# Kernel optimization log

Hardware: AMD Instinct MI355X
Metric: run time of the kernel (lower is better)

Reference implementation:

```python
import jax, jax.numpy as jnp
import numpy as np

EMBED_DIM = 528
NUM_HEADS = 8
HEAD_DIM = EMBED_DIM // NUM_HEADS  # 66


def setup_inputs() -> dict:
    key = jax.random.key(0)
    k1, k2, k3, k4, k5 = jax.random.split(key, 5)
    B, D, H, W, C = 1, 16, 16, 16, EMBED_DIM
    s = 1.0 / np.sqrt(C)
    return {
        "x": jax.random.normal(k1, (B, D, H, W, C), dtype=jnp.float32),
        "w_qkv": jax.random.uniform(k2, (3 * C, C), dtype=jnp.float32, minval=-s, maxval=s),
        "b_qkv": jax.random.uniform(k3, (3 * C,), dtype=jnp.float32, minval=-s, maxval=s),
        "w_proj": jax.random.uniform(k4, (C, C), dtype=jnp.float32, minval=-s, maxval=s),
        "b_proj": jax.random.uniform(k5, (C,), dtype=jnp.float32, minval=-s, maxval=s),
    }


def reference(x, w_qkv, b_qkv, w_proj, b_proj):
    B, D, H, W, C = x.shape
    N = D * H * W
    h, hd = NUM_HEADS, HEAD_DIM
    scaling = hd ** (-0.5)

    xt = x.reshape(B, N, C)
    # qkv projection: [B, N, 3C] -> [3, B, h, N, hd]
    qkv = xt @ w_qkv.T + b_qkv
    qkv = qkv.reshape(B, N, 3, h, hd).transpose(2, 0, 3, 1, 4)
    q, k, v = qkv[0], qkv[1], qkv[2]

    # full attention over all D*H*W tokens
    attn = jnp.einsum('bhqd,bhkd->bhqk', q, k) * scaling
    attn = jax.nn.softmax(attn, axis=-1)
    out = jnp.einsum('bhqk,bhkd->bhqd', attn, v)  # [B, h, N, hd]

    out = out.transpose(0, 2, 1, 3).reshape(B, N, h * hd)
    out = out @ w_proj.T + b_proj
    return out.reshape(B, D, H, W, C)
```

## Files before the change

### kernel.cpp

```cpp
#include <hip/hip_runtime.h>

typedef __attribute__((ext_vector_type(8))) short bf16x8;
typedef __attribute__((ext_vector_type(4))) float f32x4;
typedef __attribute__((ext_vector_type(16))) float f32x16;

#define DEV __device__ __forceinline__

static constexpr int N_TOK = 4096;
static constexpr int C     = 528;
static constexpr int NH    = 8;
static constexpr int HD    = 66;
static constexpr int HDP   = 96;
static constexpr int VD96  = 96;
static constexpr int KP    = 544;
static constexpr int NQKV  = 1584;
static constexpr int NQKVP = 1632;

DEV unsigned short f2bf(float f) {
    unsigned int u = __float_as_uint(f);
    u = (u + 0x7fffu + ((u >> 16) & 1u)) >> 16;
    return (unsigned short)u;
}
DEV float bf2f(unsigned short h) { return __uint_as_float(((unsigned int)h) << 16); }
DEV unsigned cvtpk2(float a, float b) {
    unsigned r;
    asm("v_cvt_pk_bf16_f32 %0, %1, %2" : "=v"(r) : "v"(a), "v"(b));
    return r;
}
DEV void plswap(unsigned &a, unsigned &b) {
    asm volatile("v_permlane32_swap_b32 %0, %1" : "+v"(a), "+v"(b));
}

__global__ void k_prep_all(const float* __restrict__ x, const float* __restrict__ w_qkv,
                           const float* __restrict__ w_proj,
                           unsigned short* __restrict__ xb, unsigned short* __restrict__ wqkvb,
                           unsigned short* __restrict__ whi, unsigned short* __restrict__ wlo,
                           unsigned short* __restrict__ qb, unsigned short* __restrict__ kbuf) {
    const int T0 = N_TOK * KP;
    const int T1 = T0 + NQKVP * KP;
    const int T2 = T1 + KP * KP;
    const int T3 = T2 + NH * N_TOK * (HDP - HD);
    for (int idx = blockIdx.x * 256 + threadIdx.x; idx < T3; idx += gridDim.x * 256) {
        if (idx < T0) {
            int n = idx / KP, k = idx - n * KP;
            xb[idx] = (k < C) ? f2bf(x[n * C + k]) : (unsigned short)0;
        } else if (idx < T1) {
            int j = idx - T0;
            int n = j / KP, k = j - n * KP;
            wqkvb[j] = (n < NQKV && k < C) ? f2bf(w_qkv[n * C + k]) : (unsigned short)0;
        } else if (idx < T2) {
            int j = idx - T1;
            int n = j / KP, k = j - n * KP;
            unsigned short hi = 0, lo = 0;
            if (n < C && k < C) {
                float v = w_proj[n * C + k];
                hi = f2bf(v);
                lo = f2bf(v - bf2f(hi));
            }
            whi[j] = hi; wlo[j] = lo;
        } else {
            int j = idx - T2;
            int n = j / 30, p = j - 30 * n;
            size_t a = (size_t)n * HDP + HD + p;
            qb[a] = 0; kbuf[a] = 0;
        }
    }
}

__launch_bounds__(256)
__global__ void k_gemm_qkv(const unsigned short* __restrict__ A,
                           const unsigned short* __restrict__ B,
                           const float* __restrict__ bias,
                           unsigned short* __restrict__ qb, unsigned short* __restrict__ kbuf,
                           unsigned short* __restrict__ vtmp) {
    constexpr int LDA = 40;
    __shared__ unsigned short Al[2][128 * LDA];
    __shared__ unsigned short Bl[2][96 * LDA];
    int tid = threadIdx.x, lane = tid & 63, wid = tid >> 6;
    int m0 = blockIdx.x * 128, n0 = blockIdx.y * 96;
    int wm = (wid >> 1) * 64, wn = (wid & 1) * 48;
    int arow0 = tid >> 2, arow1 = (256 + tid) >> 2, akc = (tid & 3) * 8;
    bool bhave = tid < 128;
    int brow1 = (256 + tid) >> 2;
    f32x4 acc[4][3] = {};
    bf16x8 ra0, ra1, rb0, rb1;

    ra0 = *(const bf16x8*)&A[(size_t)(m0 + arow0) * KP + akc];
    ra1 = *(const bf16x8*)&A[(size_t)(m0 + arow1) * KP + akc];
    rb0 = *(const bf16x8*)&B[(size_t)(n0 + arow0) * KP + akc];
    if (bhave) rb1 = *(const bf16x8*)&B[(size_t)(n0 + brow1) * KP + akc];
    *(bf16x8*)&Al[0][arow0 * LDA + akc] = ra0;
    *(bf16x8*)&Al[0][arow1 * LDA + akc] = ra1;
    *(bf16x8*)&Bl[0][arow0 * LDA + akc] = rb0;
    if (bhave) *(bf16x8*)&Bl[0][brow1 * LDA + akc] = rb1;
    __syncthreads();

    int kk = (lane >> 4) * 8, cc = lane & 15;
    for (int kt = 0; kt < 17; kt++) {
        int cur = kt & 1;
        if (kt < 16) {
            int k0 = (kt + 1) * 32;
            ra0 = *(const bf16x8*)&A[(size_t)(m0 + arow0) * KP + k0 + akc];
            ra1 = *(const bf16x8*)&A[(size_t)(m0 + arow1) * KP + k0 + akc];
            rb0 = *(const bf16x8*)&B[(size_t)(n0 + arow0) * KP + k0 + akc];
            if (bhave) rb1 = *(const bf16x8*)&B[(size_t)(n0 + brow1) * KP + k0 + akc];
        }
        bf16x8 af[4], bfr[3];
#pragma unroll
        for (int mi = 0; mi < 4; mi++) af[mi] = *(const bf16x8*)&Al[cur][(wm + mi * 16 + cc) * LDA + kk];
#pragma unroll
        for (int ni = 0; ni < 3; ni++) bfr[ni] = *(const bf16x8*)&Bl[cur][(wn + ni * 16 + cc) * LDA + kk];
#pragma unroll
        for (int mi = 0; mi < 4; mi++)
#pragma unroll
            for (int ni = 0; ni < 3; ni++)
                acc[mi][ni] = __builtin_amdgcn_mfma_f32_16x16x32_bf16(af[mi], bfr[ni], acc[mi][ni], 0, 0, 0);
        if (kt < 16) {
            int nxt = cur ^ 1;
            *(bf16x8*)&Al[nxt][arow0 * LDA + akc] = ra0;
            *(bf16x8*)&Al[nxt][arow1 * LDA + akc] = ra1;
            *(bf16x8*)&Bl[nxt][arow0 * LDA + akc] = rb0;
            if (bhave) *(bf16x8*)&Bl[nxt][brow1 * LDA + akc] = rb1;
        }
        __syncthreads();
    }
#pragma unroll
    for (int mi = 0; mi < 4; mi++)
#pragma unroll
        for (int ni = 0; ni < 3; ni++)
#pragma unroll
            for (int r = 0; r < 4; r++) {
                int row = m0 + wm + mi * 16 + (lane >> 4) * 4 + r;
                int col = n0 + wn + ni * 16 + cc;
                float v = acc[mi][ni][r] + (col < NQKV ? bias[col] : 0.f);
                unsigned short b = f2bf(v);
                if (col < 2 * C) {
                    int d5 = (col >= C) ? col - C : col;
                    unsigned h = (unsigned)d5 / 66u;
                    int dd = d5 - 66 * (int)h;
                    size_t a = ((size_t)h * N_TOK + row) * HDP + dd;
                    if (col >= C) kbuf[a] = b; else qb[a] = b;
                } else if (col < NQKV) {
                    vtmp[(size_t)row * C + (col - 2 * C)] = b;
                }
            }
}

__global__ void k_reshape_v(const unsigned short* __restrict__ vtmp, unsigned short* __restrict__ vt) {
    __shared__ unsigned short lt[64 * 104];
    int h = blockIdx.y, n0 = blockIdx.x * 64, tid = threadIdx.x;
#pragma unroll
    for (int i = 0; i < 24; i++) {
        int idx = i * 256 + tid;
        int ni = idx / 96, d = idx - ni * 96;
        unsigned short v = 0;
        if (d < HD) v = vtmp[(size_t)(n0 + ni) * C + h * HD + d];
        lt[ni * 104 + d] = v;
    }
    __syncthreads();
#pragma unroll
    for (int i = 0; i < 24; i++) {
        int idx = i * 256 + tid;
        int d = idx >> 6, ni = idx & 63;
        vt[((size_t)h * VD96 + d) * N_TOK + n0 + ni] = lt[ni * 104 + d];
    }
}

__launch_bounds__(512, 2)
__global__ void k_attn(const unsigned short* __restrict__ qb,
                       const unsigned short* __restrict__ kb,
                       const unsigned short* __restrict__ vt,
                       unsigned short* __restrict__ ahi,
                       unsigned short* __restrict__ alo) {
    __shared__ __align__(16) unsigned short S[128 * 128 + 96 * 128];
    int tid = threadIdx.x, lane = tid & 63, wid = tid >> 6;
    int wq = wid & 3;
    int kh = wid >> 2;
    int hi = lane >> 5, lq = lane & 31;
    int bid = blockIdx.x;
    int head = bid & 7;
    int q0 = (bid >> 3) * 128;
    const float SC2 = 0.12309149097933274f * 1.4426950408889634f;

    bf16x8 aq[6];
    {
        const unsigned short* qrow = qb + ((size_t)head * N_TOK + q0 + wq * 32 + lq) * HDP + hi * 8;
#pragma unroll
        for (int t = 0; t < 6; t++) aq[t] = *(const bf16x8*)&qrow[t * 16];
    }
    f32x16 o0 = {}, o1 = {}, o2 = {};
    float m_r = -3e38f, l_r = 0.f;

    const unsigned short* kg = kb + (size_t)head * N_TOK * HDP;
    const unsigned short* vg = vt + (size_t)head * VD96 * N_TOK;

    const unsigned short* gpK[3];
    const unsigned short* gpV[3];
    int laK[3], laV[3];
#pragma unroll
    for (int j = 0; j < 3; j++) {
        int c = j * 512 + tid;
        int row = c / 12, ch = c - row * 12;
        gpK[j] = kg + (size_t)row * HDP + ch * 8;
        laK[j] = row * 128 + ((ch ^ (row & 15)) << 3);
        int row2 = c >> 4, ch2 = c & 15;
        gpV[j] = vg + (size_t)row2 * N_TOK + ch2 * 8;
        laV[j] = 128 * 128 + row2 * 128 + ((ch2 ^ (row2 & 15)) << 3);
    }
#pragma unroll
    for (int j = 0; j < 3; j++) {
        *(bf16x8*)&S[laK[j]] = *(const bf16x8*)gpK[j];
        *(bf16x8*)&S[laV[j]] = *(const bf16x8*)gpV[j];
    }
    __syncthreads();

    for (int kt = 0; kt < 32; kt++) {
        bf16x8 gk[3], gv[3];
        if (kt < 31) {
            size_t n1 = (size_t)(kt + 1) * 128;
#pragma unroll
            for (int j = 0; j < 3; j++) {
                gk[j] = *(const bf16x8*)(gpK[j] + n1 * HDP);
                gv[j] = *(const bf16x8*)(gpV[j] + n1);
            }
        }

        f32x16 s0 = {}, s1 = {};
        {
            int r0 = kh * 64 + lq, r1 = r0 + 32;
#pragma unroll
            for (int t = 0; t < 6; t++) {
                bf16x8 ka0 = *(const bf16x8*)&S[r0 * 128 + (((2 * t + hi) ^ (r0 & 15)) << 3)];
                bf16x8 ka1 = *(const bf16x8*)&S[r1 * 128 + (((2 * t + hi) ^ (r1 & 15)) << 3)];
                s0 = __builtin_amdgcn_mfma_f32_32x32x16_bf16(ka0, aq[t], s0, 0, 0, 0);
                s1 = __builtin_amdgcn_mfma_f32_32x32x16_bf16(ka1, aq[t], s1, 0, 0, 0);
            }
        }

        float mx = s0[0];
#pragma unroll
        for (int r = 1; r < 16; r++) mx = fmaxf(mx, s0[r]);
#pragma unroll
        for (int r = 0; r < 16; r++) mx = fmaxf(mx, s1[r]);
        mx = fmaxf(mx, __shfl_xor(mx, 32, 64));
        if (!__all((mx - m_r) * SC2 <= 8.f)) {
            float mnew = fmaxf(m_r, mx);
            float fct = __builtin_amdgcn_exp2f((m_r - mnew) * SC2);
            m_r = mnew;
            l_r *= fct;
#pragma unroll
            for (int r = 0; r < 16; r++) { o0[r] *= fct; o1[r] *= fct; o2[r] *= fct; }
        }
        float nb = m_r * SC2;
        float lsum = 0.f;
#pragma unroll
        for (int r = 0; r < 16; r++) { s0[r] = __builtin_amdgcn_exp2f(__builtin_fmaf(s0[r], SC2, -nb)); lsum += s0[r]; }
#pragma unroll
        for (int r = 0; r < 16; r++) { s1[r] = __builtin_amdgcn_exp2f(__builtin_fmaf(s1[r], SC2, -nb)); lsum += s1[r]; }
        lsum += __shfl_xor(lsum, 32, 64);
        l_r += lsum;

        unsigned u0[2][4], u1[2][4];
#pragma unroll
        for (int a = 0; a < 4; a++) {
            u0[0][a] = cvtpk2(s0[4 * a + 0], s0[4 * a + 1]);
            u1[0][a] = cvtpk2(s0[4 * a + 2], s0[4 * a + 3]);
            u0[1][a] = cvtpk2(s1[4 * a + 0], s1[4 * a + 1]);
            u1[1][a] = cvtpk2(s1[4 * a + 2], s1[4 * a + 3]);
        }
#pragma unroll
        for (int kb2 = 0; kb2 < 2; kb2++)
#pragma unroll
            for (int a0 = 0; a0 < 4; a0 += 2) {
                plswap(u0[kb2][a0], u0[kb2][a0 + 1]);
                plswap(u1[kb2][a0], u1[kb2][a0 + 1]);
            }

#pragma unroll
        for (int t2 = 0; t2 < 4; t2++) {
            int kb2 = t2 >> 1, a0 = (t2 & 1) * 2;
            union { unsigned u[4]; bf16x8 v; } pf;
            pf.u[0] = u0[kb2][a0];     pf.u[1] = u1[kb2][a0];
            pf.u[2] = u0[kb2][a0 + 1]; pf.u[3] = u1[kb2][a0 + 1];
            int ch = kh * 8 + 2 * t2 + hi;
            int rv0 = lq, rv1 = 32 + lq, rv2 = 64 + lq;
            bf16x8 va0 = *(const bf16x8*)&S[128 * 128 + rv0 * 128 + ((ch ^ (rv0 & 15)) << 3)];
            bf16x8 va1 = *(const bf16x8*)&S[128 * 128 + rv1 * 128 + ((ch ^ (rv1 & 15)) << 3)];
            bf16x8 va2 = *(const bf16x8*)&S[128 * 128 + rv2 * 128 + ((ch ^ (rv2 & 15)) << 3)];
            o0 = __builtin_amdgcn_mfma_f32_32x32x16_bf16(va0, pf.v, o0, 0, 0, 0);
            o1 = __builtin_amdgcn_mfma_f32_32x32x16_bf16(va1, pf.v, o1, 0, 0, 0);
            o2 = __builtin_amdgcn_mfma_f32_32x32x16_bf16(va2, pf.v, o2, 0, 0, 0);
        }

        __syncthreads();
        if (kt < 31) {
#pragma unroll
            for (int j = 0; j < 3; j++) {
                *(bf16x8*)&S[laK[j]] = gk[j];
                *(bf16x8*)&S[laV[j]] = gv[j];
            }
        }
        __syncthreads();
    }

    float* xc = (float*)&S[0];
    float* rg = xc + (size_t)((wq * 64 + lane) * 52);
    if (kh == 1) {
#pragma unroll
        for (int r = 0; r < 16; r++) { rg[r] = o0[r]; rg[16 + r] = o1[r]; rg[32 + r] = o2[r]; }
        rg[48] = m_r; rg[49] = l_r;
    }
    __syncthreads();
    if (kh == 0) {
        float m1 = rg[48], l1 = rg[49];
        float m12 = fmaxf(m_r, m1);
        float f0 = __builtin_amdgcn_exp2f((m_r - m12) * SC2);
        float f1 = __builtin_amdgcn_exp2f((m1 - m12) * SC2);
        float inv = 1.f / (l_r * f0 + l1 * f1);
        int token = q0 + wq * 32 + lq;
#pragma unroll
        for (int db = 0; db < 3; db++) {
#pragma unroll
            for (int r = 0; r < 16; r++) {
                int d = db * 32 + (r & 3) + 8 * (r >> 2) + 4 * hi;
                if (d < HD) {
                    float own = (db == 0) ? o0[r] : (db == 1) ? o1[r] : o2[r];
                    float val = (own * f0 + rg[db * 16 + r] * f1) * inv;
                    unsigned short hb = f2bf(val);
                    float lo = val - bf2f(hb);
                    size_t a = (size_t)token * KP + head * HD + d;
                    ahi[a] = hb; alo[a] = f2bf(lo);
                }
            }
        }
    }
}

__launch_bounds__(256)
__global__ void k_gemm_proj(const unsigned short* __restrict__ Ahi_, const unsigned short* __restrict__ Alo_,
                            const unsigned short* __restrict__ Whi_, const unsigned short* __restrict__ Wlo_,
                            const float* __restrict__ bias, float* __restrict__ out) {
    constexpr int LDA = 40;
    __shared__ unsigned short Ah[2][128 * LDA], Aw[2][128 * LDA];
    __shared__ unsigned short Bh[2][64 * LDA],  Bw[2][64 * LDA];
    int tid = threadIdx.x, lane = tid & 63, wid = tid >> 6;
    int m0 = blockIdx.x * 128, n0 = blockIdx.y * 64;
    int wm = wid * 32;
    int arow0 = tid >> 2, arow1 = (256 + tid) >> 2, akc = (tid & 3) * 8;
    bool bok = (n0 + arow0) < KP;
    f32x4 acc[2][4] = {};
    bf16x8 rah0, rah1, ral0, ral1, rbh, rbl;
    const bf16x8 zero8 = {};

    rah0 = *(const bf16x8*)&Ahi_[(size_t)(m0 + arow0) * KP + akc];
    rah1 = *(const bf16x8*)&Ahi_[(size_t)(m0 + arow1) * KP + akc];
    ral0 = *(const bf16x8*)&Alo_[(size_t)(m0 + arow0) * KP + akc];
    ral1 = *(const bf16x8*)&Alo_[(size_t)(m0 + arow1) * KP + akc];
    rbh = bok ? *(const bf16x8*)&Whi_[(size_t)(n0 + arow0) * KP + akc] : zero8;
    rbl = bok ? *(const bf16x8*)&Wlo_[(size_t)(n0 + arow0) * KP + akc] : zero8;
    *(bf16x8*)&Ah[0][arow0 * LDA + akc] = rah0;
    *(bf16x8*)&Ah[0][arow1 * LDA + akc] = rah1;
    *(bf16x8*)&Aw[0][arow0 * LDA + akc] = ral0;
    *(bf16x8*)&Aw[0][arow1 * LDA + akc] = ral1;
    *(bf16x8*)&Bh[0][arow0 * LDA + akc] = rbh;
    *(bf16x8*)&Bw[0][arow0 * LDA + akc] = rbl;
    __syncthreads();

    int kk = (lane >> 4) * 8, cc = lane & 15;
    for (int kt = 0; kt < 17; kt++) {
        int cur = kt & 1;
        if (kt < 16) {
            int k0 = (kt + 1) * 32;
            rah0 = *(const bf16x8*)&Ahi_[(size_t)(m0 + arow0) * KP + k0 + akc];
            rah1 = *(const bf16x8*)&Ahi_[(size_t)(m0 + arow1) * KP + k0 + akc];
            ral0 = *(const bf16x8*)&Alo_[(size_t)(m0 + arow0) * KP + k0 + akc];
            ral1 = *(const bf16x8*)&Alo_[(size_t)(m0 + arow1) * KP + k0 + akc];
            rbh = bok ? *(const bf16x8*)&Whi_[(size_t)(n0 + arow0) * KP + k0 + akc] : zero8;
            rbl = bok ? *(const bf16x8*)&Wlo_[(size_t)(n0 + arow0) * KP + k0 + akc] : zero8;
        }
        bf16x8 ah[2], al[2], bh[4], bl[4];
#pragma unroll
        for (int mi = 0; mi < 2; mi++) {
            ah[mi] = *(const bf16x8*)&Ah[cur][(wm + mi * 16 + cc) * LDA + kk];
            al[mi] = *(const bf16x8*)&Aw[cur][(wm + mi * 16 + cc) * LDA + kk];
        }
#pragma unroll
        for (int ni = 0; ni < 4; ni++) {
            bh[ni] = *(const bf16x8*)&Bh[cur][(ni * 16 + cc) * LDA + kk];
            bl[ni] = *(const bf16x8*)&Bw[cur][(ni * 16 + cc) * LDA + kk];
        }
#pragma unroll
        for (int mi = 0; mi < 2; mi++)
#pragma unroll
            for (int ni = 0; ni < 4; ni++) {
                acc[mi][ni] = __builtin_amdgcn_mfma_f32_16x16x32_bf16(ah[mi], bh[ni], acc[mi][ni], 0, 0, 0);
                acc[mi][ni] = __builtin_amdgcn_mfma_f32_16x16x32_bf16(ah[mi], bl[ni], acc[mi][ni], 0, 0, 0);
                acc[mi][ni] = __builtin_amdgcn_mfma_f32_16x16x32_bf16(al[mi], bh[ni], acc[mi][ni], 0, 0, 0);
            }
        if (kt < 16) {
            int nxt = cur ^ 1;
            *(bf16x8*)&Ah[nxt][arow0 * LDA + akc] = rah0;
            *(bf16x8*)&Ah[nxt][arow1 * LDA + akc] = rah1;
            *(bf16x8*)&Aw[nxt][arow0 * LDA + akc] = ral0;
            *(bf16x8*)&Aw[nxt][arow1 * LDA + akc] = ral1;
            *(bf16x8*)&Bh[nxt][arow0 * LDA + akc] = rbh;
            *(bf16x8*)&Bw[nxt][arow0 * LDA + akc] = rbl;
        }
        __syncthreads();
    }
#pragma unroll
    for (int mi = 0; mi < 2; mi++)
#pragma unroll
        for (int ni = 0; ni < 4; ni++)
#pragma unroll
            for (int r = 0; r < 4; r++) {
                int row = m0 + wm + mi * 16 + (lane >> 4) * 4 + r;
                int col = n0 + ni * 16 + cc;
                if (col < C) out[(size_t)row * C + col] = acc[mi][ni][r] + bias[col];
            }
}

extern "C" void kernel_launch(void* const* d_in, const int* in_sizes, int n_in,
                              void* d_out, int out_size, void* d_ws, size_t ws_size,
                              hipStream_t stream) {
    const float* x      = (const float*)d_in[0];
    const float* w_qkv  = (const float*)d_in[1];
    const float* b_qkv  = (const float*)d_in[2];
    const float* w_proj = (const float*)d_in[3];
    const float* b_proj = (const float*)d_in[4];
    float* out = (float*)d_out;
    char* ws = (char*)d_ws;

    const size_t o_xb    = 0;
    const size_t o_wqkvb = o_xb    + 4456448;
    const size_t o_whi   = o_wqkvb + 1775616;
    const size_t o_wlo   = o_whi   + 591872;
    const size_t o_vtmp  = o_wlo   + 591872;
    const size_t o_qbf   = o_vtmp  + 4456448;
    const size_t o_kbf   = o_qbf   + 6291456;
    const size_t o_vt    = o_kbf   + 6291456;
    const size_t need    = o_vt + 6291456;
    if (ws_size < need) return;

    unsigned short* xb    = (unsigned short*)(ws + o_xb);
    unsigned short* wqkvb = (unsigned short*)(ws + o_wqkvb);
    unsigned short* whi   = (unsigned short*)(ws + o_whi);
    unsigned short* wlo   = (unsigned short*)(ws + o_wlo);
    unsigned short* vtmp  = (unsigned short*)(ws + o_vtmp);
    unsigned short* qbf   = (unsigned short*)(ws + o_qbf);
    unsigned short* kbf   = (unsigned short*)(ws + o_kbf);
    unsigned short* vt    = (unsigned short*)(ws + o_vt);
    unsigned short* ahi   = xb;
    unsigned short* alo   = vtmp;

    k_prep_all  <<<2048, 256, 0, stream>>>(x, w_qkv, w_proj, xb, wqkvb, whi, wlo, qbf, kbf);
    k_gemm_qkv  <<<dim3(N_TOK / 128, NQKVP / 96), 256, 0, stream>>>(xb, wqkvb, b_qkv, qbf, kbf, vtmp);
    k_reshape_v <<<dim3(N_TOK / 64, NH), 256, 0, stream>>>(vtmp, vt);
    k_attn      <<<dim3(256), 512, 0, stream>>>(qbf, kbf, vt, ahi, alo);
    k_gemm_proj <<<dim3(N_TOK / 128, 9), 256, 0, stream>>>(ahi, alo, whi, wlo, b_proj, out);
}
```

Baseline: 129.4 us.

## Split attention keys four ways per block with 1024 threads and 256-key tiles

The attention kernel now launches 1024-thread blocks in which four wave groups each cover a quarter of every 256-key tile, instead of two groups on 128-key tiles. The loop runs 16 iterations instead of 32, which halves the number of barrier pairs and doubles the waves resident per CU, giving more latency hiding. The partial softmax states are merged in two rounds through LDS. In exchange, LDS use grows to about 112 KB and per-thread register limits stay tight at 1024 threads.

```diff
diff --git a/kernel.cpp b/kernel.cpp
--- a/kernel.cpp
+++ b/kernel.cpp
@@ -166,13 +166,14 @@
     }
 }
 
-__launch_bounds__(512, 2)
+__launch_bounds__(1024, 1)
 __global__ void k_attn(const unsigned short* __restrict__ qb,
                        const unsigned short* __restrict__ kb,
                        const unsigned short* __restrict__ vt,
                        unsigned short* __restrict__ ahi,
                        unsigned short* __restrict__ alo) {
-    __shared__ __align__(16) unsigned short S[128 * 128 + 96 * 128];
+    __shared__ __align__(16) unsigned short S[256 * 128 + 96 * 256];
+    constexpr int VOFF = 256 * 128;
     int tid = threadIdx.x, lane = tid & 63, wid = tid >> 6;
     int wq = wid & 3;
     int kh = wid >> 2;
@@ -199,13 +200,13 @@
     int laK[3], laV[3];
 #pragma unroll
     for (int j = 0; j < 3; j++) {
-        int c = j * 512 + tid;
+        int c = j * 1024 + tid;
         int row = c / 12, ch = c - row * 12;
         gpK[j] = kg + (size_t)row * HDP + ch * 8;
         laK[j] = row * 128 + ((ch ^ (row & 15)) << 3);
-        int row2 = c >> 4, ch2 = c & 15;
+        int row2 = c >> 5, ch2 = c & 31;
         gpV[j] = vg + (size_t)row2 * N_TOK + ch2 * 8;
-        laV[j] = 128 * 128 + row2 * 128 + ((ch2 ^ (row2 & 15)) << 3);
+        laV[j] = VOFF + row2 * 256 + ((ch2 ^ (row2 & 15)) << 3);
     }
 #pragma unroll
     for (int j = 0; j < 3; j++) {
@@ -214,10 +215,10 @@
     }
     __syncthreads();
 
-    for (int kt = 0; kt < 32; kt++) {
+    for (int kt = 0; kt < 16; kt++) {
         bf16x8 gk[3], gv[3];
-        if (kt < 31) {
-            size_t n1 = (size_t)(kt + 1) * 128;
+        if (kt < 15) {
+            size_t n1 = (size_t)(kt + 1) * 256;
 #pragma unroll
             for (int j = 0; j < 3; j++) {
                 gk[j] = *(const bf16x8*)(gpK[j] + n1 * HDP);
@@ -284,16 +285,16 @@
             pf.u[2] = u0[kb2][a0 + 1]; pf.u[3] = u1[kb2][a0 + 1];
             int ch = kh * 8 + 2 * t2 + hi;
             int rv0 = lq, rv1 = 32 + lq, rv2 = 64 + lq;
-            bf16x8 va0 = *(const bf16x8*)&S[128 * 128 + rv0 * 128 + ((ch ^ (rv0 & 15)) << 3)];
-            bf16x8 va1 = *(const bf16x8*)&S[128 * 128 + rv1 * 128 + ((ch ^ (rv1 & 15)) << 3)];
-            bf16x8 va2 = *(const bf16x8*)&S[128 * 128 + rv2 * 128 + ((ch ^ (rv2 & 15)) << 3)];
+            bf16x8 va0 = *(const bf16x8*)&S[VOFF + rv0 * 256 + ((ch ^ (rv0 & 15)) << 3)];
+            bf16x8 va1 = *(const bf16x8*)&S[VOFF + rv1 * 256 + ((ch ^ (rv1 & 15)) << 3)];
+            bf16x8 va2 = *(const bf16x8*)&S[VOFF + rv2 * 256 + ((ch ^ (rv2 & 15)) << 3)];
             o0 = __builtin_amdgcn_mfma_f32_32x32x16_bf16(va0, pf.v, o0, 0, 0, 0);
             o1 = __builtin_amdgcn_mfma_f32_32x32x16_bf16(va1, pf.v, o1, 0, 0, 0);
             o2 = __builtin_amdgcn_mfma_f32_32x32x16_bf16(va2, pf.v, o2, 0, 0, 0);
         }
 
         __syncthreads();
-        if (kt < 31) {
+        if (kt < 15) {
 #pragma unroll
             for (int j = 0; j < 3; j++) {
                 *(bf16x8*)&S[laK[j]] = gk[j];
@@ -304,32 +305,58 @@
     }
 
     float* xc = (float*)&S[0];
-    float* rg = xc + (size_t)((wq * 64 + lane) * 52);
-    if (kh == 1) {
-#pragma unroll
-        for (int r = 0; r < 16; r++) { rg[r] = o0[r]; rg[16 + r] = o1[r]; rg[32 + r] = o2[r]; }
-        rg[48] = m_r; rg[49] = l_r;
-    }
-    __syncthreads();
-    if (kh == 0) {
-        float m1 = rg[48], l1 = rg[49];
-        float m12 = fmaxf(m_r, m1);
-        float f0 = __builtin_amdgcn_exp2f((m_r - m12) * SC2);
-        float f1 = __builtin_amdgcn_exp2f((m1 - m12) * SC2);
-        float inv = 1.f / (l_r * f0 + l1 * f1);
-        int token = q0 + wq * 32 + lq;
-#pragma unroll
-        for (int db = 0; db < 3; db++) {
+    {
+        float* rg = xc + (size_t)(((wq * 2 + (kh & 1)) * 64 + lane) * 52);
+        if (kh >= 2) {
+#pragma unroll
+            for (int r = 0; r < 16; r++) { rg[r] = o0[r]; rg[16 + r] = o1[r]; rg[32 + r] = o2[r]; }
+            rg[48] = m_r; rg[49] = l_r;
+        }
+        __syncthreads();
+        if (kh < 2) {
+            float m1 = rg[48], l1 = rg[49];
+            float m12 = fmaxf(m_r, m1);
+            float f0 = __builtin_amdgcn_exp2f((m_r - m12) * SC2);
+            float f1 = __builtin_amdgcn_exp2f((m1 - m12) * SC2);
+            l_r = l_r * f0 + l1 * f1;
+            m_r = m12;
 #pragma unroll
             for (int r = 0; r < 16; r++) {
-                int d = db * 32 + (r & 3) + 8 * (r >> 2) + 4 * hi;
-                if (d < HD) {
-                    float own = (db == 0) ? o0[r] : (db == 1) ? o1[r] : o2[r];
-                    float val = (own * f0 + rg[db * 16 + r] * f1) * inv;
-                    unsigned short hb = f2bf(val);
-                    float lo = val - bf2f(hb);
-                    size_t a = (size_t)token * KP + head * HD + d;
-                    ahi[a] = hb; alo[a] = f2bf(lo);
+                o0[r] = o0[r] * f0 + rg[r] * f1;
+                o1[r] = o1[r] * f0 + rg[16 + r] * f1;
+                o2[r] = o2[r] * f0 + rg[32 + r] * f1;
+            }
+        }
+        __syncthreads();
+    }
+    {
+        float* rg = xc + (size_t)((wq * 64 + lane) * 52);
+        if (kh == 1) {
+#pragma unroll
+            for (int r = 0; r < 16; r++) { rg[r] = o0[r]; rg[16 + r] = o1[r]; rg[32 + r] = o2[r]; }
+            rg[48] = m_r; rg[49] = l_r;
+        }
+        __syncthreads();
+        if (kh == 0) {
+            float m1 = rg[48], l1 = rg[49];
+            float m12 = fmaxf(m_r, m1);
+            float f0 = __builtin_amdgcn_exp2f((m_r - m12) * SC2);
+            float f1 = __builtin_amdgcn_exp2f((m1 - m12) * SC2);
+            float inv = 1.f / (l_r * f0 + l1 * f1);
+            int token = q0 + wq * 32 + lq;
+#pragma unroll
+            for (int db = 0; db < 3; db++) {
+#pragma unroll
+                for (int r = 0; r < 16; r++) {
+                    int d = db * 32 + (r & 3) + 8 * (r >> 2) + 4 * hi;
+                    if (d < HD) {
+                        float own = (db == 0) ? o0[r] : (db == 1) ? o1[r] : o2[r];
+                        float val = (own * f0 + rg[db * 16 + r] * f1) * inv;
+                        unsigned short hb = f2bf(val);
+                        float lo = val - bf2f(hb);
+                        size_t a = (size_t)token * KP + head * HD + d;
+                        ahi[a] = hb; alo[a] = f2bf(lo);
+                    }
                 }
             }
         }
@@ -456,6 +483,6 @@
     k_prep_all  <<<2048, 256, 0, stream>>>(x, w_qkv, w_proj, xb, wqkvb, whi, wlo, qbf, kbf);
     k_gemm_qkv  <<<dim3(N_TOK / 128, NQKVP / 96), 256, 0, stream>>>(xb, wqkvb, b_qkv, qbf, kbf, vtmp);
     k_reshape_v <<<dim3(N_TOK / 64, NH), 256, 0, stream>>>(vtmp, vt);
-    k_attn      <<<dim3(256), 512, 0, stream>>>(qbf, kbf, vt, ahi, alo);
+    k_attn      <<<dim3(256), 1024, 0, stream>>>(qbf, kbf, vt, ahi, alo);
     k_gemm_proj <<<dim3(N_TOK / 128, 9), 256, 0, stream>>>(ahi, alo, whi, wlo, b_proj, out);
 }
```

Measured after the change: 290.1 us. 2.24x slower.

## Split attention KV range across two blocks with atomic-ordered merge

Applied to the files above, without the earlier changes.

The attention grid doubles from 256 to 512 blocks, and each block processes half of the key/value sequence for its query tile, in the style of split-K flash decoding. The block that finishes first writes partially normalized output plus its running max and sum to a workspace. The second block spins on a flag, then merges both halves and writes the final hi/lo bf16 output. This targets underuse of the 256 compute units by the 256-block grid, at the cost of an extra global round trip, atomics, and a spin-wait that could deadlock if the partner block is never scheduled.

```diff
diff --git a/kernel.cpp b/kernel.cpp
--- a/kernel.cpp
+++ b/kernel.cpp
@@ -35,12 +35,14 @@
                            const float* __restrict__ w_proj,
                            unsigned short* __restrict__ xb, unsigned short* __restrict__ wqkvb,
                            unsigned short* __restrict__ whi, unsigned short* __restrict__ wlo,
-                           unsigned short* __restrict__ qb, unsigned short* __restrict__ kbuf) {
+                           unsigned short* __restrict__ qb, unsigned short* __restrict__ kbuf,
+                           int* __restrict__ syncb) {
     const int T0 = N_TOK * KP;
     const int T1 = T0 + NQKVP * KP;
     const int T2 = T1 + KP * KP;
     const int T3 = T2 + NH * N_TOK * (HDP - HD);
-    for (int idx = blockIdx.x * 256 + threadIdx.x; idx < T3; idx += gridDim.x * 256) {
+    const int T4 = T3 + 512;
+    for (int idx = blockIdx.x * 256 + threadIdx.x; idx < T4; idx += gridDim.x * 256) {
         if (idx < T0) {
             int n = idx / KP, k = idx - n * KP;
             xb[idx] = (k < C) ? f2bf(x[n * C + k]) : (unsigned short)0;
@@ -58,11 +60,13 @@
                 lo = f2bf(v - bf2f(hi));
             }
             whi[j] = hi; wlo[j] = lo;
-        } else {
+        } else if (idx < T3) {
             int j = idx - T2;
             int n = j / 30, p = j - 30 * n;
             size_t a = (size_t)n * HDP + HD + p;
             qb[a] = 0; kbuf[a] = 0;
+        } else {
+            syncb[idx - T3] = 0;
         }
     }
 }
@@ -171,15 +175,19 @@
                        const unsigned short* __restrict__ kb,
                        const unsigned short* __restrict__ vt,
                        unsigned short* __restrict__ ahi,
-                       unsigned short* __restrict__ alo) {
+                       unsigned short* __restrict__ alo,
+                       float* __restrict__ mlb, int* __restrict__ syncb) {
     __shared__ __align__(16) unsigned short S[128 * 128 + 96 * 128];
+    __shared__ int role_sh;
     int tid = threadIdx.x, lane = tid & 63, wid = tid >> 6;
     int wq = wid & 3;
     int kh = wid >> 2;
     int hi = lane >> 5, lq = lane & 31;
     int bid = blockIdx.x;
     int head = bid & 7;
-    int q0 = (bid >> 3) * 128;
+    int q0 = ((bid >> 3) & 31) * 128;
+    int kvh = bid >> 8;
+    int pid = bid & 255;
     const float SC2 = 0.12309149097933274f * 1.4426950408889634f;
 
     bf16x8 aq[6];
@@ -191,8 +199,8 @@
     f32x16 o0 = {}, o1 = {}, o2 = {};
     float m_r = -3e38f, l_r = 0.f;
 
-    const unsigned short* kg = kb + (size_t)head * N_TOK * HDP;
-    const unsigned short* vg = vt + (size_t)head * VD96 * N_TOK;
+    const unsigned short* kg = kb + ((size_t)head * N_TOK + kvh * 2048) * HDP;
+    const unsigned short* vg = vt + (size_t)head * VD96 * N_TOK + kvh * 2048;
 
     const unsigned short* gpK[3];
     const unsigned short* gpV[3];
@@ -214,9 +222,9 @@
     }
     __syncthreads();
 
-    for (int kt = 0; kt < 32; kt++) {
+    for (int kt = 0; kt < 16; kt++) {
         bf16x8 gk[3], gv[3];
-        if (kt < 31) {
+        if (kt < 15) {
             size_t n1 = (size_t)(kt + 1) * 128;
 #pragma unroll
             for (int j = 0; j < 3; j++) {
@@ -293,7 +301,7 @@
         }
 
         __syncthreads();
-        if (kt < 31) {
+        if (kt < 15) {
 #pragma unroll
             for (int j = 0; j < 3; j++) {
                 *(bf16x8*)&S[laK[j]] = gk[j];
@@ -316,20 +324,68 @@
         float m12 = fmaxf(m_r, m1);
         float f0 = __builtin_amdgcn_exp2f((m_r - m12) * SC2);
         float f1 = __builtin_amdgcn_exp2f((m1 - m12) * SC2);
-        float inv = 1.f / (l_r * f0 + l1 * f1);
-        int token = q0 + wq * 32 + lq;
-#pragma unroll
-        for (int db = 0; db < 3; db++) {
-#pragma unroll
-            for (int r = 0; r < 16; r++) {
-                int d = db * 32 + (r & 3) + 8 * (r >> 2) + 4 * hi;
-                if (d < HD) {
-                    float own = (db == 0) ? o0[r] : (db == 1) ? o1[r] : o2[r];
-                    float val = (own * f0 + rg[db * 16 + r] * f1) * inv;
-                    unsigned short hb = f2bf(val);
-                    float lo = val - bf2f(hb);
-                    size_t a = (size_t)token * KP + head * HD + d;
-                    ahi[a] = hb; alo[a] = f2bf(lo);
+        l_r = l_r * f0 + l1 * f1;
+        m_r = m12;
+#pragma unroll
+        for (int r = 0; r < 16; r++) {
+            o0[r] = o0[r] * f0 + rg[r] * f1;
+            o1[r] = o1[r] * f0 + rg[16 + r] * f1;
+            o2[r] = o2[r] * f0 + rg[32 + r] * f1;
+        }
+    }
+
+    if (tid == 0) role_sh = atomicAdd(&syncb[pid], 1);
+    __syncthreads();
+    int role = role_sh;
+    int token = q0 + wq * 32 + lq;
+    if (role == 0) {
+        if (kh == 0) {
+#pragma unroll
+            for (int db = 0; db < 3; db++) {
+#pragma unroll
+                for (int r = 0; r < 16; r++) {
+                    int d = db * 32 + (r & 3) + 8 * (r >> 2) + 4 * hi;
+                    if (d < HD) {
+                        float val = (db == 0) ? o0[r] : (db == 1) ? o1[r] : o2[r];
+                        unsigned short hb = f2bf(val);
+                        size_t a = (size_t)token * KP + head * HD + d;
+                        ahi[a] = hb; alo[a] = f2bf(val - bf2f(hb));
+                    }
+                }
+            }
+            if (hi == 0) {
+                size_t mli = ((size_t)(kvh * 8 + head) * 4096 + token) * 2;
+                mlb[mli] = m_r; mlb[mli + 1] = l_r;
+            }
+        }
+        __syncthreads();
+        if (tid == 0) { __threadfence(); atomicExch(&syncb[256 + pid], 1); }
+    } else {
+        if (tid == 0) {
+            while (atomicAdd(&syncb[256 + pid], 0) == 0) {}
+            __threadfence();
+        }
+        __syncthreads();
+        if (kh == 0) {
+            size_t mlo = ((size_t)((1 - kvh) * 8 + head) * 4096 + token) * 2;
+            float m_o = mlb[mlo], l_o = mlb[mlo + 1];
+            float fm = fmaxf(m_r, m_o);
+            float f_m = __builtin_amdgcn_exp2f((m_r - fm) * SC2);
+            float f_o = __builtin_amdgcn_exp2f((m_o - fm) * SC2);
+            float inv = 1.f / (l_r * f_m + l_o * f_o);
+#pragma unroll
+            for (int db = 0; db < 3; db++) {
+#pragma unroll
+                for (int r = 0; r < 16; r++) {
+                    int d = db * 32 + (r & 3) + 8 * (r >> 2) + 4 * hi;
+                    if (d < HD) {
+                        float own = (db == 0) ? o0[r] : (db == 1) ? o1[r] : o2[r];
+                        size_t a = (size_t)token * KP + head * HD + d;
+                        float Oo = bf2f(ahi[a]) + bf2f(alo[a]);
+                        float val = (own * f_m + Oo * f_o) * inv;
+                        unsigned short hb = f2bf(val);
+                        ahi[a] = hb; alo[a] = f2bf(val - bf2f(hb));
+                    }
                 }
             }
         }
@@ -439,7 +495,9 @@
     const size_t o_qbf   = o_vtmp  + 4456448;
     const size_t o_kbf   = o_qbf   + 6291456;
     const size_t o_vt    = o_kbf   + 6291456;
-    const size_t need    = o_vt + 6291456;
+    const size_t o_ml    = o_vt    + 6291456;
+    const size_t o_sync  = o_ml    + 524288;
+    const size_t need    = o_sync  + 2048;
     if (ws_size < need) return;
 
     unsigned short* xb    = (unsigned short*)(ws + o_xb);
@@ -450,12 +508,14 @@
     unsigned short* qbf   = (unsigned short*)(ws + o_qbf);
     unsigned short* kbf   = (unsigned short*)(ws + o_kbf);
     unsigned short* vt    = (unsigned short*)(ws + o_vt);
+    float*          mlb   = (float*)(ws + o_ml);
+    int*            syncb = (int*)(ws + o_sync);
     unsigned short* ahi   = xb;
     unsigned short* alo   = vtmp;
 
-    k_prep_all  <<<2048, 256, 0, stream>>>(x, w_qkv, w_proj, xb, wqkvb, whi, wlo, qbf, kbf);
+    k_prep_all  <<<2048, 256, 0, stream>>>(x, w_qkv, w_proj, xb, wqkvb, whi, wlo, qbf, kbf, syncb);
     k_gemm_qkv  <<<dim3(N_TOK / 128, NQKVP / 96), 256, 0, stream>>>(xb, wqkvb, b_qkv, qbf, kbf, vtmp);
     k_reshape_v <<<dim3(N_TOK / 64, NH), 256, 0, stream>>>(vtmp, vt);
-    k_attn      <<<dim3(256), 512, 0, stream>>>(qbf, kbf, vt, ahi, alo);
+    k_attn      <<<dim3(512), 512, 0, stream>>>(qbf, kbf, vt, ahi, alo, mlb, syncb);
     k_gemm_proj <<<dim3(N_TOK / 128, 9), 256, 0, stream>>>(ahi, alo, whi, wlo, b_proj, out);
 }
```

New measurement: 158.4 us. 22.3% more time.

## Double-buffer K/V tiles in LDS and drop one barrier per iteration

Applied to the files above, without the earlier changes.

Splits shared memory into two K and two V buffers so the next tile is written to the alternate buffer without a preceding barrier, leaving one __syncthreads per iteration. Also raises wave priority around MFMA blocks, hoists half the V fragment LDS loads before the softmax, and splits the max/sum reductions into four independent chains. Doubling LDS use may cut the number of resident blocks per CU below the launch-bounds target, reducing latency hiding.

```diff
diff --git a/kernel.cpp b/kernel.cpp
--- a/kernel.cpp
+++ b/kernel.cpp
@@ -172,7 +172,8 @@
                        const unsigned short* __restrict__ vt,
                        unsigned short* __restrict__ ahi,
                        unsigned short* __restrict__ alo) {
-    __shared__ __align__(16) unsigned short S[128 * 128 + 96 * 128];
+    __shared__ __align__(16) unsigned short Kl[2][128 * 128];
+    __shared__ __align__(16) unsigned short Vl[2][96 * 128];
     int tid = threadIdx.x, lane = tid & 63, wid = tid >> 6;
     int wq = wid & 3;
     int kh = wid >> 2;
@@ -205,16 +206,20 @@
         laK[j] = row * 128 + ((ch ^ (row & 15)) << 3);
         int row2 = c >> 4, ch2 = c & 15;
         gpV[j] = vg + (size_t)row2 * N_TOK + ch2 * 8;
-        laV[j] = 128 * 128 + row2 * 128 + ((ch2 ^ (row2 & 15)) << 3);
+        laV[j] = row2 * 128 + ((ch2 ^ (row2 & 15)) << 3);
     }
 #pragma unroll
     for (int j = 0; j < 3; j++) {
-        *(bf16x8*)&S[laK[j]] = *(const bf16x8*)gpK[j];
-        *(bf16x8*)&S[laV[j]] = *(const bf16x8*)gpV[j];
+        *(bf16x8*)&Kl[0][laK[j]] = *(const bf16x8*)gpK[j];
+        *(bf16x8*)&Vl[0][laV[j]] = *(const bf16x8*)gpV[j];
     }
     __syncthreads();
 
+    int r0 = kh * 64 + lq, r1 = r0 + 32;
+    int rv0 = lq, rv1 = 32 + lq, rv2 = 64 + lq;
+
     for (int kt = 0; kt < 32; kt++) {
+        int cur = kt & 1;
         bf16x8 gk[3], gv[3];
         if (kt < 31) {
             size_t n1 = (size_t)(kt + 1) * 128;
@@ -224,24 +229,39 @@
                 gv[j] = *(const bf16x8*)(gpV[j] + n1);
             }
         }
+        const unsigned short* Kc = &Kl[cur][0];
+        const unsigned short* Vc = &Vl[cur][0];
 
         f32x16 s0 = {}, s1 = {};
-        {
-            int r0 = kh * 64 + lq, r1 = r0 + 32;
-#pragma unroll
-            for (int t = 0; t < 6; t++) {
-                bf16x8 ka0 = *(const bf16x8*)&S[r0 * 128 + (((2 * t + hi) ^ (r0 & 15)) << 3)];
-                bf16x8 ka1 = *(const bf16x8*)&S[r1 * 128 + (((2 * t + hi) ^ (r1 & 15)) << 3)];
-                s0 = __builtin_amdgcn_mfma_f32_32x32x16_bf16(ka0, aq[t], s0, 0, 0, 0);
-                s1 = __builtin_amdgcn_mfma_f32_32x32x16_bf16(ka1, aq[t], s1, 0, 0, 0);
-            }
-        }
-
-        float mx = s0[0];
-#pragma unroll
-        for (int r = 1; r < 16; r++) mx = fmaxf(mx, s0[r]);
-#pragma unroll
-        for (int r = 0; r < 16; r++) mx = fmaxf(mx, s1[r]);
+        __builtin_amdgcn_s_setprio(1);
+#pragma unroll
+        for (int t = 0; t < 6; t++) {
+            bf16x8 ka0 = *(const bf16x8*)&Kc[r0 * 128 + (((2 * t + hi) ^ (r0 & 15)) << 3)];
+            bf16x8 ka1 = *(const bf16x8*)&Kc[r1 * 128 + (((2 * t + hi) ^ (r1 & 15)) << 3)];
+            s0 = __builtin_amdgcn_mfma_f32_32x32x16_bf16(ka0, aq[t], s0, 0, 0, 0);
+            s1 = __builtin_amdgcn_mfma_f32_32x32x16_bf16(ka1, aq[t], s1, 0, 0, 0);
+        }
+        __builtin_amdgcn_s_setprio(0);
+
+        bf16x8 hv[6];
+#pragma unroll
+        for (int t2 = 0; t2 < 2; t2++) {
+            int ch = kh * 8 + 2 * t2 + hi;
+            hv[t2 * 3 + 0] = *(const bf16x8*)&Vc[rv0 * 128 + ((ch ^ (rv0 & 15)) << 3)];
+            hv[t2 * 3 + 1] = *(const bf16x8*)&Vc[rv1 * 128 + ((ch ^ (rv1 & 15)) << 3)];
+            hv[t2 * 3 + 2] = *(const bf16x8*)&Vc[rv2 * 128 + ((ch ^ (rv2 & 15)) << 3)];
+        }
+
+        float ma = fmaxf(s0[0], s1[0]), mb = fmaxf(s0[1], s1[1]);
+        float mc = fmaxf(s0[2], s1[2]), md = fmaxf(s0[3], s1[3]);
+#pragma unroll
+        for (int r = 4; r < 16; r += 4) {
+            ma = fmaxf(ma, fmaxf(s0[r + 0], s1[r + 0]));
+            mb = fmaxf(mb, fmaxf(s0[r + 1], s1[r + 1]));
+            mc = fmaxf(mc, fmaxf(s0[r + 2], s1[r + 2]));
+            md = fmaxf(md, fmaxf(s0[r + 3], s1[r + 3]));
+        }
+        float mx = fmaxf(fmaxf(ma, mb), fmaxf(mc, md));
         mx = fmaxf(mx, __shfl_xor(mx, 32, 64));
         if (!__all((mx - m_r) * SC2 <= 8.f)) {
             float mnew = fmaxf(m_r, mx);
@@ -252,11 +272,22 @@
             for (int r = 0; r < 16; r++) { o0[r] *= fct; o1[r] *= fct; o2[r] *= fct; }
         }
         float nb = m_r * SC2;
-        float lsum = 0.f;
-#pragma unroll
-        for (int r = 0; r < 16; r++) { s0[r] = __builtin_amdgcn_exp2f(__builtin_fmaf(s0[r], SC2, -nb)); lsum += s0[r]; }
-#pragma unroll
-        for (int r = 0; r < 16; r++) { s1[r] = __builtin_amdgcn_exp2f(__builtin_fmaf(s1[r], SC2, -nb)); lsum += s1[r]; }
+        float la = 0.f, lb = 0.f, lc = 0.f, ld = 0.f;
+#pragma unroll
+        for (int r = 0; r < 16; r += 4) {
+            s0[r + 0] = __builtin_amdgcn_exp2f(__builtin_fmaf(s0[r + 0], SC2, -nb)); la += s0[r + 0];
+            s0[r + 1] = __builtin_amdgcn_exp2f(__builtin_fmaf(s0[r + 1], SC2, -nb)); lb += s0[r + 1];
+            s0[r + 2] = __builtin_amdgcn_exp2f(__builtin_fmaf(s0[r + 2], SC2, -nb)); lc += s0[r + 2];
+            s0[r + 3] = __builtin_amdgcn_exp2f(__builtin_fmaf(s0[r + 3], SC2, -nb)); ld += s0[r + 3];
+        }
+#pragma unroll
+        for (int r = 0; r < 16; r += 4) {
+            s1[r + 0] = __builtin_amdgcn_exp2f(__builtin_fmaf(s1[r + 0], SC2, -nb)); la += s1[r + 0];
+            s1[r + 1] = __builtin_amdgcn_exp2f(__builtin_fmaf(s1[r + 1], SC2, -nb)); lb += s1[r + 1];
+            s1[r + 2] = __builtin_amdgcn_exp2f(__builtin_fmaf(s1[r + 2], SC2, -nb)); lc += s1[r + 2];
+            s1[r + 3] = __builtin_amdgcn_exp2f(__builtin_fmaf(s1[r + 3], SC2, -nb)); ld += s1[r + 3];
+        }
+        float lsum = (la + lb) + (lc + ld);
         lsum += __shfl_xor(lsum, 32, 64);
         l_r += lsum;
 
@@ -276,34 +307,40 @@
                 plswap(u1[kb2][a0], u1[kb2][a0 + 1]);
             }
 
+        __builtin_amdgcn_s_setprio(1);
 #pragma unroll
         for (int t2 = 0; t2 < 4; t2++) {
             int kb2 = t2 >> 1, a0 = (t2 & 1) * 2;
             union { unsigned u[4]; bf16x8 v; } pf;
             pf.u[0] = u0[kb2][a0];     pf.u[1] = u1[kb2][a0];
             pf.u[2] = u0[kb2][a0 + 1]; pf.u[3] = u1[kb2][a0 + 1];
-            int ch = kh * 8 + 2 * t2 + hi;
-            int rv0 = lq, rv1 = 32 + lq, rv2 = 64 + lq;
-            bf16x8 va0 = *(const bf16x8*)&S[128 * 128 + rv0 * 128 + ((ch ^ (rv0 & 15)) << 3)];
-            bf16x8 va1 = *(const bf16x8*)&S[128 * 128 + rv1 * 128 + ((ch ^ (rv1 & 15)) << 3)];
-            bf16x8 va2 = *(const bf16x8*)&S[128 * 128 + rv2 * 128 + ((ch ^ (rv2 & 15)) << 3)];
+            bf16x8 va0, va1, va2;
+            if (t2 < 2) {
+                va0 = hv[t2 * 3 + 0]; va1 = hv[t2 * 3 + 1]; va2 = hv[t2 * 3 + 2];
+            } else {
+                int ch = kh * 8 + 2 * t2 + hi;
+                va0 = *(const bf16x8*)&Vc[rv0 * 128 + ((ch ^ (rv0 & 15)) << 3)];
+                va1 = *(const bf16x8*)&Vc[rv1 * 128 + ((ch ^ (rv1 & 15)) << 3)];
+                va2 = *(const bf16x8*)&Vc[rv2 * 128 + ((ch ^ (rv2 & 15)) << 3)];
+            }
             o0 = __builtin_amdgcn_mfma_f32_32x32x16_bf16(va0, pf.v, o0, 0, 0, 0);
             o1 = __builtin_amdgcn_mfma_f32_32x32x16_bf16(va1, pf.v, o1, 0, 0, 0);
             o2 = __builtin_amdgcn_mfma_f32_32x32x16_bf16(va2, pf.v, o2, 0, 0, 0);
         }
-
+        __builtin_amdgcn_s_setprio(0);
+
+        if (kt < 31) {
+            int nxt = cur ^ 1;
+#pragma unroll
+            for (int j = 0; j < 3; j++) {
+                *(bf16x8*)&Kl[nxt][laK[j]] = gk[j];
+                *(bf16x8*)&Vl[nxt][laV[j]] = gv[j];
+            }
+        }
         __syncthreads();
-        if (kt < 31) {
-#pragma unroll
-            for (int j = 0; j < 3; j++) {
-                *(bf16x8*)&S[laK[j]] = gk[j];
-                *(bf16x8*)&S[laV[j]] = gv[j];
-            }
-        }
-        __syncthreads();
-    }
-
-    float* xc = (float*)&S[0];
+    }
+
+    float* xc = (float*)&Kl[0][0];
     float* rg = xc + (size_t)((wq * 64 + lane) * 52);
     if (kh == 1) {
 #pragma unroll
```

Result: no change. 129.7 us (+0.2%).
